# Kernel tuning notes

Hardware: AMD Instinct MI355X
Metric: run time of the kernel (lower is better)

## Reference

```python
import jax, jax.numpy as jnp
import numpy as np

N = 50000      # nodes
E = 800000     # edges
DIN = 256
DH = 256
DOUT = 64


def setup_inputs() -> dict:
    key = jax.random.key(0)
    ks = jax.random.split(key, 8)
    x = jax.random.normal(ks[0], (N, DIN), dtype=jnp.float32)
    edge_index = jax.random.randint(ks[1], (2, E), 0, N, dtype=jnp.int64)
    s = 0.05
    W1 = jax.random.normal(ks[2], (DIN, DH), dtype=jnp.float32) * s
    b1 = jnp.zeros((DH,), dtype=jnp.float32)
    W2 = jax.random.normal(ks[3], (DH, DH), dtype=jnp.float32) * s
    b2 = jnp.zeros((DH,), dtype=jnp.float32)
    W3 = jax.random.normal(ks[4], (DH, DOUT), dtype=jnp.float32) * s
    b3 = jnp.zeros((DOUT,), dtype=jnp.float32)
    return {"x": x, "edge_index": edge_index, "W1": W1, "b1": b1,
            "W2": W2, "b2": b2, "W3": W3, "b3": b3}


def gcn_conv(x, src, dst, deg_inv_sqrt, W, b):
    # x: [N, din] -> [N, dout]. PyG GCNConv: h = D^{-1/2}(A+I)D^{-1/2} (x W) + b
    n = x.shape[0]
    h = x @ W                                   # [N, dout]
    norm = deg_inv_sqrt[src] * deg_inv_sqrt[dst]  # [E+N]
    msgs = h[src] * norm[:, None]               # gather + scale, [E+N, dout]
    out = jax.ops.segment_sum(msgs, dst, num_segments=n)  # scatter-add
    return out + b


def _loops(edge_index, n):
    # add self loops, compute symmetric normalization degrees
    sl = jnp.arange(n, dtype=edge_index.dtype)
    src = jnp.concatenate([edge_index[0], sl])
    dst = jnp.concatenate([edge_index[1], sl])
    deg = jax.ops.segment_sum(jnp.ones_like(dst, dtype=jnp.float32), dst, num_segments=n)
    dis = jnp.where(deg > 0, jax.lax.rsqrt(deg), 0.0)
    return src, dst, dis


def reference(x, edge_index, W1, b1, W2, b2, W3, b3):
    src, dst, dis = _loops(edge_index, x.shape[0])
    h = jax.nn.relu(gcn_conv(x, src, dst, dis, W1, b1))   # dropout: eval no-op
    h = jax.nn.relu(gcn_conv(h, src, dst, dis, W2, b2))
    out = gcn_conv(h, src, dst, dis, W3, b3)              # batch=None -> no pooling
    return out
```

## Files before the change

kernel.cpp:

```cpp
#include <hip/hip_runtime.h>
#include <hip/hip_fp8.h>
#include <cstdint>
#include <cstddef>

typedef unsigned short u16;
typedef _Float16 f16x8 __attribute__((ext_vector_type(8)));
typedef float f32x2 __attribute__((ext_vector_type(2)));
typedef float f32x4 __attribute__((ext_vector_type(4)));

#if defined(__has_builtin)
#if __has_builtin(__builtin_amdgcn_cvt_pk_f32_fp8) && __has_builtin(__builtin_amdgcn_cvt_pk_fp8_f32)
#define FP8_BUILTIN 1
#endif
#endif

__device__ __forceinline__ float h2f(u16 u) {
  return (float)__builtin_bit_cast(_Float16, u);
}
__device__ __forceinline__ u16 f2h(float f) {
  return __builtin_bit_cast(u16, (_Float16)f);
}
__device__ __forceinline__ unsigned pkh(float lo, float hi) {
  return (unsigned)f2h(lo) | ((unsigned)f2h(hi) << 16);
}
__device__ __forceinline__ unsigned char ftofp8(float f) {
#ifdef FP8_BUILTIN
  return (unsigned char)(__builtin_amdgcn_cvt_pk_fp8_f32(f, f, 0, false) & 0xFF);
#else
  return __hip_fp8_e4m3(f).__x;
#endif
}

__device__ __forceinline__ void async16(u16* lds, const u16* g) {
  __builtin_amdgcn_global_load_lds(
      (const __attribute__((address_space(1))) unsigned int*)g,
      (__attribute__((address_space(3))) unsigned int*)lds, 16, 0, 0);
}

__device__ __forceinline__ void fma8p(float* a, float d, uint2 p) {
#ifdef FP8_BUILTIN
  f32x2 v0 = __builtin_amdgcn_cvt_pk_f32_fp8((int)p.x, false);
  f32x2 v1 = __builtin_amdgcn_cvt_pk_f32_fp8((int)p.x, true);
  f32x2 v2 = __builtin_amdgcn_cvt_pk_f32_fp8((int)p.y, false);
  f32x2 v3 = __builtin_amdgcn_cvt_pk_f32_fp8((int)p.y, true);
  a[0] += d * v0.x; a[1] += d * v0.y; a[2] += d * v1.x; a[3] += d * v1.y;
  a[4] += d * v2.x; a[5] += d * v2.y; a[6] += d * v3.x; a[7] += d * v3.y;
#else
  const unsigned char* b = (const unsigned char*)&p;
#pragma unroll
  for (int k = 0; k < 8; ++k) {
    __hip_fp8_e4m3 v; v.__x = b[k];
    a[k] += d * (float)v;
  }
#endif
}

__device__ __forceinline__ void fma16p(float* a, float d, uint4 p) {
  fma8p(a, d, make_uint2(p.x, p.y));
  fma8p(a + 8, d, make_uint2(p.z, p.w));
}

__device__ __forceinline__ void fma8h(float* a, float d, uint4 p) {
  const u16* q = (const u16*)&p;
#pragma unroll
  for (int k = 0; k < 8; ++k) a[k] += d * h2f(q[k]);
}

__device__ __forceinline__ f16x8 cvt8(const float* p) {
  float4 a = *(const float4*)p;
  float4 b = *(const float4*)(p + 4);
  f16x8 r;
  r[0] = (_Float16)a.x; r[1] = (_Float16)a.y; r[2] = (_Float16)a.z; r[3] = (_Float16)a.w;
  r[4] = (_Float16)b.x; r[5] = (_Float16)b.y; r[6] = (_Float16)b.z; r[7] = (_Float16)b.w;
  return r;
}

__device__ __forceinline__ int wave_is64(const void* ep) {
  const unsigned* p = (const unsigned*)ep;
  const int lane = threadIdx.x & 63;
  unsigned v = p[2 * lane + 1] | p[2 * (lane + 64) + 1];
  unsigned long long bal = __ballot(v != 0u);
  return (bal == 0ull) ? 1 : 0;
}

__device__ __forceinline__ int edge_at(const void* ep, int is64, long long idx) {
  if (is64) return (int)((const long long*)ep)[idx];
  return ((const int*)ep)[idx];
}

#define NCHUNK 256

__global__ void zero_f32(float* p, int n) {
  int i = blockIdx.x * 256 + threadIdx.x;
  if (i < n) p[i] = 0.f;
}

__global__ __launch_bounds__(256) void prep_all(
    const float* __restrict__ W1, u16* __restrict__ wt1,
    const float* __restrict__ W2, u16* __restrict__ wt2,
    const float* __restrict__ W3, u16* __restrict__ wt3,
    const void* __restrict__ ep, int* __restrict__ cnt,
    int E, int N, int DIN, int DH, int DOUT,
    int nb_w1, int nb_w2, int nb_w3) {
  int b = blockIdx.x;
  if (b < nb_w1) {
    int idx = b * 256 + threadIdx.x;
    if (idx < DIN * DH) {
      int n = idx / DIN, k = idx % DIN;
      wt1[idx] = f2h(W1[k * DH + n]);
    }
    return;
  }
  b -= nb_w1;
  if (b < nb_w2) {
    int idx = b * 256 + threadIdx.x;
    if (idx < DH * DH) {
      int n = idx / DH, k = idx % DH;
      wt2[idx] = f2h(W2[k * DH + n]);
    }
    return;
  }
  b -= nb_w2;
  if (b < nb_w3) {
    int idx = b * 256 + threadIdx.x;
    if (idx < DH * DOUT) {
      int n = idx / DH, k = idx % DH;
      wt3[idx] = f2h(W3[k * DOUT + n]);
    }
    return;
  }
  b -= nb_w3;
  {
    __shared__ int h[256];
    h[threadIdx.x] = 0;
    __syncthreads();
    int is64 = wave_is64(ep);
    const int per = (E + NCHUNK - 1) / NCHUNK;
    const int e0 = b * per, e1 = min(e0 + per, E);
    for (int e = e0 + (int)threadIdx.x; e < e1; e += 256) {
      int d = edge_at(ep, is64, (long long)E + e);
      d = min(max(d, 0), N - 1);
      atomicAdd(&h[d >> 8], 1);
    }
    __syncthreads();
    cnt[b * 256 + threadIdx.x] = h[threadIdx.x];
  }
}

__device__ __forceinline__ void bases_in_lds(const int* __restrict__ cnt,
                                             int nbuck, int E, int* bl, int* ws4) {
  const int t = threadIdx.x, lane = t & 63, w = t >> 6;
  int tot = 0;
  if (t < nbuck) {
#pragma unroll 4
    for (int c = 0; c < NCHUNK; ++c) tot += cnt[c * 256 + t];
  }
  int inc = tot;
#pragma unroll
  for (int o = 1; o < 64; o <<= 1) {
    int u = __shfl_up(inc, o, 64);
    if (lane >= o) inc += u;
  }
  if (lane == 63) ws4[w] = inc;
  __syncthreads();
  if (t == 0) {
    int run = 0;
#pragma unroll
    for (int k = 0; k < 4; ++k) { int v = ws4[k]; ws4[k + 4] = run; run += v; }
  }
  __syncthreads();
  bl[t] = ws4[w + 4] + inc - tot;
  if (t == 0) bl[nbuck] = E;
  __syncthreads();
}

template <int BN, int OUT8, int A32, int NBT, int SC>
__device__ __forceinline__ void gemm_dev(const void* __restrict__ A,
                                         const u16* __restrict__ Bt,
                                         void* __restrict__ Cv, int Nt,
                                         int Nrows, int bm, int col0, u16* Bs) {
  constexpr int K = 256;
  constexpr int NJ = BN / 16;
  constexpr int CH = BN * K / 8;
  const int tid = threadIdx.x, lane = tid & 63, w = tid >> 6;

  auto stage = [&](int bt) {
#pragma unroll
    for (int i = 0; i < CH / 256; ++i) {
      int c = tid + i * 256;
      int ln = c & 63, t2 = c >> 6;
      int ks = t2 & 7, j = t2 >> 3;
      int row = bt * BN + j * 16 + (ln & 15);
      int kk = ks * 32 + (ln >> 4) * 8;
      async16(&Bs[(size_t)c * 8], Bt + (size_t)row * K + kk);
    }
  };
  stage(0);

  const int r16 = lane & 15, quad = lane >> 4;
  const int m0 = w * 32;
  int row0 = bm * 128 + m0 + r16;
  int row1 = row0 + 16;
  f16x8 aa0[8], aa1[8];
  if (A32) {
    row0 = min(row0, Nrows - 1);
    row1 = min(row1, Nrows - 1);
    const float* A0 = (const float*)A + (size_t)row0 * K + quad * 8;
    const float* A1 = (const float*)A + (size_t)row1 * K + quad * 8;
#pragma unroll
    for (int ks = 0; ks < 8; ++ks) {
      aa0[ks] = cvt8(A0 + ks * 32);
      aa1[ks] = cvt8(A1 + ks * 32);
    }
  } else {
    const u16* A0 = (const u16*)A + (size_t)row0 * K + quad * 8;
    const u16* A1 = (const u16*)A + (size_t)row1 * K + quad * 8;
#pragma unroll
    for (int ks = 0; ks < 8; ++ks) {
      aa0[ks] = *(const f16x8*)(A0 + ks * 32);
      aa1[ks] = *(const f16x8*)(A1 + ks * 32);
    }
  }

  const f32x4 fzero = {0.f, 0.f, 0.f, 0.f};
#pragma unroll
  for (int bt = 0; bt < NBT; ++bt) {
    f32x4 acc[2][NJ];
#pragma unroll
    for (int i = 0; i < 2; ++i)
#pragma unroll
      for (int j = 0; j < NJ; ++j) acc[i][j] = fzero;
    __syncthreads();
#pragma unroll
    for (int ks = 0; ks < 8; ++ks)
#pragma unroll
      for (int j = 0; j < NJ; ++j) {
        f16x8 bf = *(const f16x8*)(&Bs[(size_t)((j * 8 + ks) * 64 + lane) * 8]);
        acc[0][j] = __builtin_amdgcn_mfma_f32_16x16x32_f16(aa0[ks], bf, acc[0][j], 0, 0, 0);
        acc[1][j] = __builtin_amdgcn_mfma_f32_16x16x32_f16(aa1[ks], bf, acc[1][j], 0, 0, 0);
      }
    if (bt + 1 < NBT) {
      __syncthreads();
      stage(bt + 1);
    }
#pragma unroll
    for (int i = 0; i < 2; ++i)
#pragma unroll
      for (int j = 0; j < NJ; ++j) {
        int gr = bm * 128 + m0 + i * 16 + quad * 4;
        int gc = col0 + bt * BN + j * 16 + r16;
#pragma unroll
        for (int r = 0; r < 4; ++r) {
          if (OUT8) {
            ((unsigned char*)Cv)[(size_t)(gr + r) * Nt + gc] =
                ftofp8(acc[i][j][r] * (float)SC);
          } else {
            ((u16*)Cv)[(size_t)(gr + r) * Nt + gc] = f2h(acc[i][j][r]);
          }
        }
      }
  }
}

template <int BN, int OUT8, int A32, int NBT, int SC>
__global__ __launch_bounds__(256) void gemm_bres(const void* __restrict__ A,
                                                 const u16* __restrict__ Bt,
                                                 void* __restrict__ Cv, int Nt,
                                                 int Nrows) {
  __shared__ __align__(16) u16 Bs[BN * 256];
  const int col0 = blockIdx.y * (NBT * BN);
  gemm_dev<BN, OUT8, A32, NBT, SC>(A, Bt + (size_t)col0 * 256, Cv, Nt, Nrows,
                                   (int)blockIdx.x, col0, Bs);
}

__global__ __launch_bounds__(256) void bucket_gemm1(
    const void* __restrict__ ep, const int* __restrict__ cnt,
    unsigned* __restrict__ tmp, const float* __restrict__ x,
    const u16* __restrict__ wt1, unsigned char* __restrict__ hbuf,
    int E, int N, int nbuck) {
  __shared__ __align__(16) u16 Bs[128 * 256];
  if ((int)blockIdx.x >= NCHUNK) {
    gemm_dev<128, 1, 1, 2, 1>(x, wt1, hbuf, 256, N, (int)blockIdx.x - NCHUNK, 0, Bs);
    return;
  }
  int* bl = (int*)Bs;
  int* cur = bl + 272;
  int* ws4 = cur + 256;
  const int chunk = blockIdx.x;
  const int t = threadIdx.x;
  bases_in_lds(cnt, nbuck, E, bl, ws4);
  if (t < nbuck) {
    int partial = 0;
    for (int c = 0; c < chunk; ++c) partial += cnt[c * 256 + t];
    cur[t] = bl[t] + partial;
  }
  __syncthreads();
  int is64 = wave_is64(ep);
  const int per = (E + NCHUNK - 1) / NCHUNK;
  const int e0 = chunk * per, e1 = min(e0 + per, E);
  for (int e = e0 + t; e < e1; e += 256) {
    int s = edge_at(ep, is64, e);
    int d = edge_at(ep, is64, (long long)E + e);
    s = min(max(s, 0), N - 1);
    d = min(max(d, 0), N - 1);
    int pos = atomicAdd(&cur[d >> 8], 1);
    tmp[pos] = ((unsigned)d << 16) | (unsigned)s;
  }
}

__global__ __launch_bounds__(256) void csr_final(const unsigned* __restrict__ tmp,
                                                 const int* __restrict__ cnt,
                                                 int* __restrict__ rp,
                                                 float* __restrict__ dis,
                                                 u16* __restrict__ col,
                                                 int N, int E, int nbuck) {
  __shared__ int bl[257];
  __shared__ int hcnt[256];
  __shared__ int curs[256];
  __shared__ int ws4[8];
  const int b = blockIdx.x;
  const int node0 = b * 256;
  const int t = threadIdx.x, lane = t & 63, w = t >> 6;
  bases_in_lds(cnt, nbuck, E, bl, ws4);
  const int k0 = bl[b], k1 = bl[b + 1];
  hcnt[t] = 0;
  __syncthreads();
  for (int k = k0 + t; k < k1; k += 256)
    atomicAdd(&hcnt[(int)(tmp[k] >> 16) - node0], 1);
  __syncthreads();
  const int v = hcnt[t];
  int inc = v;
#pragma unroll
  for (int o = 1; o < 64; o <<= 1) {
    int u = __shfl_up(inc, o, 64);
    if (lane >= o) inc += u;
  }
  __syncthreads();
  if (lane == 63) ws4[w] = inc;
  __syncthreads();
  if (t == 0) {
    int run = 0;
#pragma unroll
    for (int k = 0; k < 4; ++k) { int vv = ws4[k]; ws4[k + 4] = run; run += vv; }
  }
  __syncthreads();
  const int excl = k0 + ws4[w + 4] + inc - v;
  if (node0 + t < N) {
    rp[node0 + t] = excl;
    dis[node0 + t] = rsqrtf((float)(v + 1));
  }
  if (b == 0 && t == 0) rp[N] = E;
  curs[t] = excl;
  __syncthreads();
  for (int k = k0 + t; k < k1; k += 256) {
    unsigned e = tmp[k];
    int dl = (int)(e >> 16) - node0;
    int pos = atomicAdd(&curs[dl], 1);
    col[pos] = (u16)(e & 0xFFFFu);
  }
}

template <int SCALED>
__global__ __launch_bounds__(256) void agg_d256(const unsigned char* __restrict__ h,
                                                const int* __restrict__ rp,
                                                const u16* __restrict__ col,
                                                const float* __restrict__ dis,
                                                const float* __restrict__ bias,
                                                u16* __restrict__ out, int N) {
  const int wid = threadIdx.x >> 6, lane = threadIdx.x & 63;
  const int i = blockIdx.x * 4 + wid;
  if (i >= N) return;
  const int sub = lane >> 4;
  const int l16 = lane & 15;
  const int cb = l16 * 16;
  const float di = dis[i];
  float a[16];
#pragma unroll
  for (int k = 0; k < 16; ++k) a[k] = 0.f;
  if (sub == 0) {
    uint4 sv = *(const uint4*)(h + (size_t)i * 256 + cb);
    fma16p(a, SCALED ? 1.f : di, sv);
  }
  const int e1 = rp[i + 1];
  for (int base = rp[i]; base < e1; base += 64) {
    int me = base + lane;
    int s_l = 0; float d_l = 0.f;
    if (me < e1) { s_l = (int)col[me]; if (!SCALED) d_l = dis[s_l]; }
    const int cnt = min(64, e1 - base);
    const int cntR = (cnt + 15) & ~15;
    for (int t = 0; t < cntR; t += 16) {
      int sA = __shfl(s_l, t + sub, 64);
      int sB = __shfl(s_l, t + 4 + sub, 64);
      int sC = __shfl(s_l, t + 8 + sub, 64);
      int sD = __shfl(s_l, t + 12 + sub, 64);
      float dA, dB, dC, dD;
      if (SCALED) {
        dA = (t + sub < cnt) ? 1.f : 0.f;
        dB = (t + 4 + sub < cnt) ? 1.f : 0.f;
        dC = (t + 8 + sub < cnt) ? 1.f : 0.f;
        dD = (t + 12 + sub < cnt) ? 1.f : 0.f;
      } else {
        dA = __shfl(d_l, t + sub, 64);
        dB = __shfl(d_l, t + 4 + sub, 64);
        dC = __shfl(d_l, t + 8 + sub, 64);
        dD = __shfl(d_l, t + 12 + sub, 64);
      }
      uint4 pA = *(const uint4*)(h + (size_t)sA * 256 + cb);
      uint4 pB = *(const uint4*)(h + (size_t)sB * 256 + cb);
      uint4 pC = *(const uint4*)(h + (size_t)sC * 256 + cb);
      uint4 pD = *(const uint4*)(h + (size_t)sD * 256 + cb);
      fma16p(a, dA, pA); fma16p(a, dB, pB); fma16p(a, dC, pC); fma16p(a, dD, pD);
    }
  }
#pragma unroll
  for (int k = 0; k < 16; ++k) a[k] += __shfl_xor(a[k], 16, 64);
#pragma unroll
  for (int k = 0; k < 16; ++k) a[k] += __shfl_xor(a[k], 32, 64);
  if (sub == 0) {
    const float inv = SCALED ? 0.25f : 1.f;
    const float* bp = bias + l16 * 16;
    float4 b0 = *(const float4*)(bp);
    float4 b1 = *(const float4*)(bp + 4);
    float4 b2 = *(const float4*)(bp + 8);
    float4 b3 = *(const float4*)(bp + 12);
    float bb[16] = {b0.x, b0.y, b0.z, b0.w, b1.x, b1.y, b1.z, b1.w,
                    b2.x, b2.y, b2.z, b2.w, b3.x, b3.y, b3.z, b3.w};
    float r[16];
#pragma unroll
    for (int k = 0; k < 16; ++k)
      r[k] = fmaxf(di * a[k] * inv + bb[k], 0.f) * di;
    uint4 o0, o1;
    o0.x = pkh(r[0], r[1]);  o0.y = pkh(r[2], r[3]);
    o0.z = pkh(r[4], r[5]);  o0.w = pkh(r[6], r[7]);
    o1.x = pkh(r[8], r[9]);  o1.y = pkh(r[10], r[11]);
    o1.z = pkh(r[12], r[13]); o1.w = pkh(r[14], r[15]);
    *(uint4*)(out + (size_t)i * 256 + l16 * 16) = o0;
    *(uint4*)(out + (size_t)i * 256 + l16 * 16 + 8) = o1;
  }
}

__global__ __launch_bounds__(256) void agg_d64(const u16* __restrict__ h,
                                               const int* __restrict__ rp,
                                               const u16* __restrict__ col,
                                               const float* __restrict__ dis,
                                               const float* __restrict__ bias,
                                               float* __restrict__ out, int N) {
  const int wid = threadIdx.x >> 6, lane = threadIdx.x & 63;
  const int i = blockIdx.x * 4 + wid;
  if (i >= N) return;
  const int grp = lane >> 3;
  const int l8 = lane & 7;
  const int c8 = l8 * 8;
  const float di = dis[i];
  float a[8] = {0.f, 0.f, 0.f, 0.f, 0.f, 0.f, 0.f, 0.f};
  if (grp == 0) {
    uint4 sv = *(const uint4*)(h + (size_t)i * 64 + c8);
    fma8h(a, 1.f, sv);
  }
  const int e1 = rp[i + 1];
  for (int base = rp[i]; base < e1; base += 64) {
    int me = base + lane;
    int s_l = 0;
    if (me < e1) s_l = (int)col[me];
    const int cnt = min(64, e1 - base);
    const int cntR = (cnt + 15) & ~15;
    for (int t = 0; t < cntR; t += 16) {
      int sA = __shfl(s_l, t + grp, 64);
      int sB = __shfl(s_l, t + 8 + grp, 64);
      float dA = (t + grp < cnt) ? 1.f : 0.f;
      float dB = (t + 8 + grp < cnt) ? 1.f : 0.f;
      uint4 pA = *(const uint4*)(h + (size_t)sA * 64 + c8);
      uint4 pB = *(const uint4*)(h + (size_t)sB * 64 + c8);
      fma8h(a, dA, pA); fma8h(a, dB, pB);
    }
  }
#pragma unroll
  for (int k = 0; k < 8; ++k) a[k] += __shfl_xor(a[k], 8, 64);
#pragma unroll
  for (int k = 0; k < 8; ++k) a[k] += __shfl_xor(a[k], 16, 64);
#pragma unroll
  for (int k = 0; k < 8; ++k) a[k] += __shfl_xor(a[k], 32, 64);
  if (lane < 8) {
    float4 b0 = *(const float4*)(bias + c8);
    float4 b1 = *(const float4*)(bias + c8 + 4);
    float4 o0, o1;
    o0.x = di * a[0] + b0.x; o0.y = di * a[1] + b0.y;
    o0.z = di * a[2] + b0.z; o0.w = di * a[3] + b0.w;
    o1.x = di * a[4] + b1.x; o1.y = di * a[5] + b1.y;
    o1.z = di * a[6] + b1.z; o1.w = di * a[7] + b1.w;
    *(float4*)(out + (size_t)i * 64 + c8) = o0;
    *(float4*)(out + (size_t)i * 64 + c8 + 4) = o1;
  }
}

extern "C" void kernel_launch(void* const* d_in, const int* in_sizes, int n_in,
                              void* d_out, int out_size, void* d_ws, size_t ws_size,
                              hipStream_t stream) {
  if (n_in < 8) return;
  const float* x = (const float*)d_in[0];
  const void* eptr = d_in[1];
  const float* W1 = (const float*)d_in[2];
  const float* b1 = (const float*)d_in[3];
  const float* W2 = (const float*)d_in[4];
  const float* b2 = (const float*)d_in[5];
  const float* W3 = (const float*)d_in[6];
  const float* b3 = (const float*)d_in[7];
  float* out = (float*)d_out;

  const int DIN = 256, DH = 256;
  const int N = in_sizes[0] / DIN;
  const int E = in_sizes[1] / 2;
  const int DOUT = in_sizes[6] / DH;
  const int MT = (N + 127) / 128;
  const int Mpad = MT * 128;
  const int nbuck = (N + 255) >> 8;

  auto rnd = [](size_t b) { return (b + 255) & ~(size_t)255; };
  size_t required = 0;
  required += rnd((size_t)Mpad * DH * 2);
  required += rnd((size_t)Mpad * DH);
  required += rnd((size_t)E * 2);
  required += rnd((size_t)E * 4);
  required += rnd((size_t)(N + 1) * 4);
  required += rnd((size_t)N * 4);
  required += rnd((size_t)DIN * DH * 2);
  required += rnd((size_t)DH * DH * 2);
  required += rnd((size_t)DH * DOUT * 2);
  required += rnd((size_t)256 * NCHUNK * 4);
  if (ws_size < required || N > 65536 || nbuck > 256 || nbuck < 1 ||
      E < 128 || DOUT != 64) {
    zero_f32<<<(out_size + 255) / 256, 256, 0, stream>>>(out, out_size);
    return;
  }

  char* ws = (char*)d_ws;
  size_t off0 = 0;
  auto alloc = [&](size_t bytes) {
    char* p = ws + off0;
    off0 = (off0 + bytes + 255) & ~(size_t)255;
    return p;
  };
  u16* xpad = (u16*)alloc((size_t)Mpad * DH * 2);
  unsigned char* hbuf = (unsigned char*)alloc((size_t)Mpad * DH);
  u16* colb = (u16*)alloc((size_t)E * 2);
  unsigned* tmpb = (unsigned*)alloc((size_t)E * 4);
  int* rp = (int*)alloc((size_t)(N + 1) * 4);
  float* dis = (float*)alloc((size_t)N * 4);
  u16* wt1 = (u16*)alloc((size_t)DIN * DH * 2);
  u16* wt2 = (u16*)alloc((size_t)DH * DH * 2);
  u16* wt3 = (u16*)alloc((size_t)DH * DOUT * 2);
  int* cnt = (int*)alloc((size_t)256 * NCHUNK * 4);

  const int nb_w1 = (DIN * DH + 255) / 256;
  const int nb_w2 = (DH * DH + 255) / 256;
  const int nb_w3 = (DH * DOUT + 255) / 256;
  prep_all<<<nb_w1 + nb_w2 + nb_w3 + NCHUNK, 256, 0, stream>>>(
      W1, wt1, W2, wt2, W3, wt3, eptr, cnt,
      E, N, DIN, DH, DOUT, nb_w1, nb_w2, nb_w3);

  bucket_gemm1<<<NCHUNK + MT, 256, 0, stream>>>(eptr, cnt, tmpb, x, wt1, hbuf,
                                                E, N, nbuck);
  csr_final<<<nbuck, 256, 0, stream>>>(tmpb, cnt, rp, dis, colb, N, E, nbuck);

  agg_d256<0><<<(N + 3) / 4, 256, 0, stream>>>(hbuf, rp, colb, dis, b1, xpad, N);
  gemm_bres<128, 1, 0, 2, 4><<<dim3(MT, 1), 256, 0, stream>>>(xpad, wt2, hbuf, DH, N);
  agg_d256<1><<<(N + 3) / 4, 256, 0, stream>>>(hbuf, rp, colb, dis, b2, xpad, N);
  gemm_bres<64, 0, 0, 1, 1><<<dim3(MT, DOUT / 64), 256, 0, stream>>>(
      xpad, wt3, hbuf, DOUT, N);
  agg_d64<<<(N + 3) / 4, 256, 0, stream>>>((const u16*)hbuf, rp, colb, dis, b3,
                                           out, N);
}
```

Measured before the change: 323.7 us.

## Shrink GEMM B tile to 64 columns and halve aggregation unroll with packed FMA

```diff
diff --git a/kernel.cpp b/kernel.cpp
--- a/kernel.cpp
+++ b/kernel.cpp
@@ -37,27 +37,27 @@
       (__attribute__((address_space(3))) unsigned int*)lds, 16, 0, 0);
 }
 
-__device__ __forceinline__ void fma8p(float* a, float d, uint2 p) {
+__device__ __forceinline__ void fma8p2(f32x2* a2, float d, uint2 p) {
 #ifdef FP8_BUILTIN
+  f32x2 d2; d2[0] = d; d2[1] = d;
   f32x2 v0 = __builtin_amdgcn_cvt_pk_f32_fp8((int)p.x, false);
   f32x2 v1 = __builtin_amdgcn_cvt_pk_f32_fp8((int)p.x, true);
   f32x2 v2 = __builtin_amdgcn_cvt_pk_f32_fp8((int)p.y, false);
   f32x2 v3 = __builtin_amdgcn_cvt_pk_f32_fp8((int)p.y, true);
-  a[0] += d * v0.x; a[1] += d * v0.y; a[2] += d * v1.x; a[3] += d * v1.y;
-  a[4] += d * v2.x; a[5] += d * v2.y; a[6] += d * v3.x; a[7] += d * v3.y;
+  a2[0] += d2 * v0; a2[1] += d2 * v1; a2[2] += d2 * v2; a2[3] += d2 * v3;
 #else
   const unsigned char* b = (const unsigned char*)&p;
 #pragma unroll
   for (int k = 0; k < 8; ++k) {
     __hip_fp8_e4m3 v; v.__x = b[k];
-    a[k] += d * (float)v;
+    a2[k >> 1][k & 1] += d * (float)v;
   }
 #endif
 }
 
-__device__ __forceinline__ void fma16p(float* a, float d, uint4 p) {
-  fma8p(a, d, make_uint2(p.x, p.y));
-  fma8p(a + 8, d, make_uint2(p.z, p.w));
+__device__ __forceinline__ void fma16p2(f32x2* a2, float d, uint4 p) {
+  fma8p2(a2, d, make_uint2(p.x, p.y));
+  fma8p2(a2 + 4, d, make_uint2(p.z, p.w));
 }
 
 __device__ __forceinline__ void fma8h(float* a, float d, uint4 p) {
@@ -174,14 +174,16 @@
   __syncthreads();
 }
 
-template <int BN, int OUT8, int A32, int NBT, int SC>
-__device__ __forceinline__ void gemm_dev(const void* __restrict__ A,
-                                         const u16* __restrict__ Bt,
-                                         void* __restrict__ Cv, int Nt,
-                                         int Nrows, int bm, int col0, u16* Bs) {
+template <int OUT8, int A32, int NBT, int SC>
+__device__ __forceinline__ void gemm64_dev(const void* __restrict__ A,
+                                           const u16* __restrict__ Bt,
+                                           void* __restrict__ Cv, int Nt,
+                                           int Nrows, int bm, u16* Bs) {
   constexpr int K = 256;
-  constexpr int NJ = BN / 16;
+  constexpr int BN = 64;
+  constexpr int NJ = 4;
   constexpr int CH = BN * K / 8;
+
   const int tid = threadIdx.x, lane = tid & 63, w = tid >> 6;
 
   auto stage = [&](int bt) {
@@ -248,7 +250,7 @@
 #pragma unroll
       for (int j = 0; j < NJ; ++j) {
         int gr = bm * 128 + m0 + i * 16 + quad * 4;
-        int gc = col0 + bt * BN + j * 16 + r16;
+        int gc = bt * BN + j * 16 + r16;
 #pragma unroll
         for (int r = 0; r < 4; ++r) {
           if (OUT8) {
@@ -262,15 +264,13 @@
   }
 }
 
-template <int BN, int OUT8, int A32, int NBT, int SC>
-__global__ __launch_bounds__(256) void gemm_bres(const void* __restrict__ A,
-                                                 const u16* __restrict__ Bt,
-                                                 void* __restrict__ Cv, int Nt,
-                                                 int Nrows) {
-  __shared__ __align__(16) u16 Bs[BN * 256];
-  const int col0 = blockIdx.y * (NBT * BN);
-  gemm_dev<BN, OUT8, A32, NBT, SC>(A, Bt + (size_t)col0 * 256, Cv, Nt, Nrows,
-                                   (int)blockIdx.x, col0, Bs);
+template <int OUT8, int A32, int NBT, int SC>
+__global__ __launch_bounds__(256) void gemm64c(const void* __restrict__ A,
+                                               const u16* __restrict__ Bt,
+                                               void* __restrict__ Cv, int Nt,
+                                               int Nrows) {
+  __shared__ __align__(16) u16 Bs[64 * 256];
+  gemm64_dev<OUT8, A32, NBT, SC>(A, Bt, Cv, Nt, Nrows, (int)blockIdx.x, Bs);
 }
 
 __global__ __launch_bounds__(256) void bucket_gemm1(
@@ -278,9 +278,9 @@
     unsigned* __restrict__ tmp, const float* __restrict__ x,
     const u16* __restrict__ wt1, unsigned char* __restrict__ hbuf,
     int E, int N, int nbuck) {
-  __shared__ __align__(16) u16 Bs[128 * 256];
+  __shared__ __align__(16) u16 Bs[64 * 256];
   if ((int)blockIdx.x >= NCHUNK) {
-    gemm_dev<128, 1, 1, 2, 1>(x, wt1, hbuf, 256, N, (int)blockIdx.x - NCHUNK, 0, Bs);
+    gemm64_dev<1, 1, 4, 1>(x, wt1, hbuf, 256, N, (int)blockIdx.x - NCHUNK, Bs);
     return;
   }
   int* bl = (int*)Bs;
@@ -374,48 +374,46 @@
   const int l16 = lane & 15;
   const int cb = l16 * 16;
   const float di = dis[i];
-  float a[16];
-#pragma unroll
-  for (int k = 0; k < 16; ++k) a[k] = 0.f;
+  f32x2 a2[8];
+#pragma unroll
+  for (int k = 0; k < 8; ++k) { a2[k][0] = 0.f; a2[k][1] = 0.f; }
   if (sub == 0) {
     uint4 sv = *(const uint4*)(h + (size_t)i * 256 + cb);
-    fma16p(a, SCALED ? 1.f : di, sv);
+    fma16p2(a2, SCALED ? 1.f : di, sv);
   }
   const int e1 = rp[i + 1];
   for (int base = rp[i]; base < e1; base += 64) {
-    int me = base + lane;
+    const int me = base + lane;
     int s_l = 0; float d_l = 0.f;
     if (me < e1) { s_l = (int)col[me]; if (!SCALED) d_l = dis[s_l]; }
     const int cnt = min(64, e1 - base);
-    const int cntR = (cnt + 15) & ~15;
-    for (int t = 0; t < cntR; t += 16) {
+    const int cntR = (cnt + 7) & ~7;
+    for (int t = 0; t < cntR; t += 8) {
       int sA = __shfl(s_l, t + sub, 64);
       int sB = __shfl(s_l, t + 4 + sub, 64);
-      int sC = __shfl(s_l, t + 8 + sub, 64);
-      int sD = __shfl(s_l, t + 12 + sub, 64);
-      float dA, dB, dC, dD;
+      float dA, dB;
       if (SCALED) {
         dA = (t + sub < cnt) ? 1.f : 0.f;
         dB = (t + 4 + sub < cnt) ? 1.f : 0.f;
-        dC = (t + 8 + sub < cnt) ? 1.f : 0.f;
-        dD = (t + 12 + sub < cnt) ? 1.f : 0.f;
       } else {
         dA = __shfl(d_l, t + sub, 64);
         dB = __shfl(d_l, t + 4 + sub, 64);
-        dC = __shfl(d_l, t + 8 + sub, 64);
-        dD = __shfl(d_l, t + 12 + sub, 64);
       }
       uint4 pA = *(const uint4*)(h + (size_t)sA * 256 + cb);
       uint4 pB = *(const uint4*)(h + (size_t)sB * 256 + cb);
-      uint4 pC = *(const uint4*)(h + (size_t)sC * 256 + cb);
-      uint4 pD = *(const uint4*)(h + (size_t)sD * 256 + cb);
-      fma16p(a, dA, pA); fma16p(a, dB, pB); fma16p(a, dC, pC); fma16p(a, dD, pD);
-    }
-  }
-#pragma unroll
-  for (int k = 0; k < 16; ++k) a[k] += __shfl_xor(a[k], 16, 64);
-#pragma unroll
-  for (int k = 0; k < 16; ++k) a[k] += __shfl_xor(a[k], 32, 64);
+      fma16p2(a2, dA, pA); fma16p2(a2, dB, pB);
+    }
+  }
+#pragma unroll
+  for (int k = 0; k < 8; ++k) {
+    a2[k][0] += __shfl_xor(a2[k][0], 16, 64);
+    a2[k][1] += __shfl_xor(a2[k][1], 16, 64);
+  }
+#pragma unroll
+  for (int k = 0; k < 8; ++k) {
+    a2[k][0] += __shfl_xor(a2[k][0], 32, 64);
+    a2[k][1] += __shfl_xor(a2[k][1], 32, 64);
+  }
   if (sub == 0) {
     const float inv = SCALED ? 0.25f : 1.f;
     const float* bp = bias + l16 * 16;
@@ -428,7 +426,7 @@
     float r[16];
 #pragma unroll
     for (int k = 0; k < 16; ++k)
-      r[k] = fmaxf(di * a[k] * inv + bb[k], 0.f) * di;
+      r[k] = fmaxf(di * a2[k >> 1][k & 1] * inv + bb[k], 0.f) * di;
     uint4 o0, o1;
     o0.x = pkh(r[0], r[1]);  o0.y = pkh(r[2], r[3]);
     o0.z = pkh(r[4], r[5]);  o0.w = pkh(r[6], r[7]);
@@ -562,11 +560,11 @@
                                                 E, N, nbuck);
   csr_final<<<nbuck, 256, 0, stream>>>(tmpb, cnt, rp, dis, colb, N, E, nbuck);
 
-  agg_d256<0><<<(N + 3) / 4, 256, 0, stream>>>(hbuf, rp, colb, dis, b1, xpad, N);
-  gemm_bres<128, 1, 0, 2, 4><<<dim3(MT, 1), 256, 0, stream>>>(xpad, wt2, hbuf, DH, N);
-  agg_d256<1><<<(N + 3) / 4, 256, 0, stream>>>(hbuf, rp, colb, dis, b2, xpad, N);
-  gemm_bres<64, 0, 0, 1, 1><<<dim3(MT, DOUT / 64), 256, 0, stream>>>(
-      xpad, wt3, hbuf, DOUT, N);
-  agg_d64<<<(N + 3) / 4, 256, 0, stream>>>((const u16*)hbuf, rp, colb, dis, b3,
-                                           out, N);
-}
+  const int gb = (N + 3) / 4;
+
+  agg_d256<0><<<gb, 256, 0, stream>>>(hbuf, rp, colb, dis, b1, xpad, N);
+  gemm64c<1, 0, 4, 4><<<MT, 256, 0, stream>>>(xpad, wt2, hbuf, DH, N);
+  agg_d256<1><<<gb, 256, 0, stream>>>(hbuf, rp, colb, dis, b2, xpad, N);
+  gemm64c<0, 0, 1, 1><<<MT, 256, 0, stream>>>(xpad, wt3, hbuf, DOUT, N);
+  agg_d64<<<gb, 256, 0, stream>>>((const u16*)hbuf, rp, colb, dis, b3, out, N);
+}
```

Result: faster. 283.0 us (median of 4 runs) (-12.6%).
